# Performance work log

Hardware: AMD Instinct MI355X
Metric: run time of the kernel (lower is better)

Reference implementation:

```python
import jax, jax.numpy as jnp
import numpy as np

NUM_NEURONS = 8192
INPUT_SIZE = 512
OUTPUT_SIZE = 512
TAU = 10.0
G = 1.5


def setup_inputs() -> dict:
    key = jax.random.key(0)
    k1, k2, k3, k4, k5 = jax.random.split(key, 5)
    inputs = jax.random.normal(k1, (INPUT_SIZE,), dtype=jnp.float32)
    potentials = jax.random.normal(k2, (1, NUM_NEURONS), dtype=jnp.float32)
    # parameters, matching the torch init scales
    W_in = jax.random.normal(k3, (INPUT_SIZE, NUM_NEURONS), dtype=jnp.float32) * 0.1
    synapses = jax.random.normal(k4, (NUM_NEURONS, NUM_NEURONS), dtype=jnp.float32) / np.sqrt(NUM_NEURONS).astype(np.float32)
    W_out = jax.random.normal(k5, (NUM_NEURONS, OUTPUT_SIZE), dtype=jnp.float32) / np.float32(NUM_NEURONS)
    return {"inputs": inputs, "potentials": potentials, "W_in": W_in,
            "synapses": synapses, "W_out": W_out}


def reference(inputs, potentials, W_in, synapses, W_out):
    # input_map: bias-free linear, then unsqueeze to [1, N]
    drive = (inputs @ W_in)[None, :]                      # [1, N]
    # Neurons: continuous-time leaky integrator (FORCE-style)
    rates = jnp.tanh(potentials)                          # [1, N]
    pot_new = potentials + (-potentials + G * (rates @ synapses) + drive) / TAU
    gen_net = jnp.tanh(pot_new)                           # [1, N]
    # read_out: bias-free linear
    output = gen_net @ W_out                              # [1, output_size]
    return (output, pot_new)
```

## Files before the change

### kernel.cpp

```cpp
#include <hip/hip_runtime.h>
#include <math.h>

#define N_NEU   8192
#define IN_SZ   512
#define OUT_SZ  512
constexpr float TAU_INV = 0.1f;
constexpr float G_GAIN  = 1.5f;

__global__ void init_kernel(const float* __restrict__ pot,
                            float* __restrict__ rates,
                            float* __restrict__ drive,
                            float* __restrict__ y,
                            float* __restrict__ out_head) {
    int j = blockIdx.x * blockDim.x + threadIdx.x;
    if (j < N_NEU) {
        float p = pot[j];
        rates[j] = tanhf(p);
        drive[j] = 0.0f;
        y[j]     = 0.0f;
    }
    if (j < OUT_SZ) out_head[j] = 0.0f;
}

template<int KPB>
__global__ void gemv_acc(const float* __restrict__ x,
                         const float* __restrict__ M,
                         float* __restrict__ y,
                         int n4) {
    __shared__ float xs[KPB];
    const int k0 = blockIdx.y * KPB;
    for (int t = threadIdx.x; t < KPB; t += blockDim.x) xs[t] = x[k0 + t];
    __syncthreads();

    const int col4 = blockIdx.x * blockDim.x + threadIdx.x;
    const float4* Mp = (const float4*)M + (size_t)k0 * n4 + col4;

    float4 acc = make_float4(0.f, 0.f, 0.f, 0.f);
#pragma unroll 8
    for (int i = 0; i < KPB; ++i) {
        float  s = xs[i];
        float4 m = Mp[(size_t)i * n4];
        acc.x = fmaf(s, m.x, acc.x);
        acc.y = fmaf(s, m.y, acc.y);
        acc.z = fmaf(s, m.z, acc.z);
        acc.w = fmaf(s, m.w, acc.w);
    }

    float* yp = y + (size_t)col4 * 4;
    atomicAdd(yp + 0, acc.x);
    atomicAdd(yp + 1, acc.y);
    atomicAdd(yp + 2, acc.z);
    atomicAdd(yp + 3, acc.w);
}

__global__ void finalize_kernel(const float* __restrict__ pot,
                                const float* __restrict__ y,
                                const float* __restrict__ drive,
                                float* __restrict__ pot_out,
                                float* __restrict__ gen) {
    int j = blockIdx.x * blockDim.x + threadIdx.x;
    float p  = pot[j];
    float pn = p + (-p + G_GAIN * y[j] + drive[j]) * TAU_INV;
    pot_out[j] = pn;
    gen[j]     = tanhf(pn);
}

extern "C" void kernel_launch(void* const* d_in, const int* in_sizes, int n_in,
                              void* d_out, int out_size, void* d_ws, size_t ws_size,
                              hipStream_t stream) {
    const float* inputs   = (const float*)d_in[0];
    const float* pot      = (const float*)d_in[1];
    const float* W_in     = (const float*)d_in[2];
    const float* synapses = (const float*)d_in[3];
    const float* W_out    = (const float*)d_in[4];

    float* out = (float*)d_out;

    float* ws_rates = (float*)d_ws;
    float* ws_drive = ws_rates + N_NEU;
    float* ws_y     = ws_drive + N_NEU;
    float* ws_gen   = ws_y     + N_NEU;

    init_kernel<<<dim3(N_NEU / 256), dim3(256), 0, stream>>>(
        pot, ws_rates, ws_drive, ws_y, out);

    gemv_acc<16><<<dim3(N_NEU / 4 / 256, IN_SZ / 16), dim3(256), 0, stream>>>(
        inputs, W_in, ws_drive, N_NEU / 4);

    gemv_acc<128><<<dim3(N_NEU / 4 / 256, N_NEU / 128), dim3(256), 0, stream>>>(
        ws_rates, synapses, ws_y, N_NEU / 4);

    finalize_kernel<<<dim3(N_NEU / 256), dim3(256), 0, stream>>>(
        pot, ws_y, ws_drive, out + OUT_SZ, ws_gen);

    gemv_acc<32><<<dim3(1, N_NEU / 32), dim3(128), 0, stream>>>(
        ws_gen, W_out, out, OUT_SZ / 4);
}
```

Before: 419.0 us.

## Fuse pipeline into two kernels with merged W_in/synapse GEMV and fused finalize-readout

Collapses five launches into two memsets plus two kernels. The first kernel runs the W_in and synapse GEMVs in one grid, computing the scaled tanh rates inline and summing both into a single accumulator. The second kernel recomputes the potential update and tanh per block, then does the W_out readout and writes pot_new, with no intermediate gen buffer. This cuts launch overhead and round trips to intermediate buffers, and changes the synapse K-split (128→64), which doubles the number of atomics.

After: 407.6 us. 1.03x faster.

```diff
diff --git a/kernel.cpp b/kernel.cpp
--- a/kernel.cpp
+++ b/kernel.cpp
@@ -4,65 +4,97 @@
 #define N_NEU   8192
 #define IN_SZ   512
 #define OUT_SZ  512
+#define N4      (N_NEU / 4)
+#define KPB     64
 constexpr float TAU_INV = 0.1f;
 constexpr float G_GAIN  = 1.5f;
 
-__global__ void init_kernel(const float* __restrict__ pot,
-                            float* __restrict__ rates,
-                            float* __restrict__ drive,
-                            float* __restrict__ y,
-                            float* __restrict__ out_head) {
-    int j = blockIdx.x * blockDim.x + threadIdx.x;
-    if (j < N_NEU) {
-        float p = pot[j];
-        rates[j] = tanhf(p);
-        drive[j] = 0.0f;
-        y[j]     = 0.0f;
+__global__ __launch_bounds__(256)
+void accum_kernel(const float* __restrict__ pot,
+                  const float* __restrict__ inputs,
+                  const float* __restrict__ synapses,
+                  const float* __restrict__ W_in,
+                  float* __restrict__ acc_buf) {
+    __shared__ float xs[KPB];
+    const int by = blockIdx.y;
+    const float4* M;
+    int k0;
+    if (by < N_NEU / KPB) {
+        k0 = by * KPB;
+        M  = (const float4*)synapses;
+        if (threadIdx.x < KPB)
+            xs[threadIdx.x] = G_GAIN * tanhf(pot[k0 + threadIdx.x]);
+    } else {
+        k0 = (by - N_NEU / KPB) * KPB;
+        M  = (const float4*)W_in;
+        if (threadIdx.x < KPB)
+            xs[threadIdx.x] = inputs[k0 + threadIdx.x];
     }
-    if (j < OUT_SZ) out_head[j] = 0.0f;
-}
-
-template<int KPB>
-__global__ void gemv_acc(const float* __restrict__ x,
-                         const float* __restrict__ M,
-                         float* __restrict__ y,
-                         int n4) {
-    __shared__ float xs[KPB];
-    const int k0 = blockIdx.y * KPB;
-    for (int t = threadIdx.x; t < KPB; t += blockDim.x) xs[t] = x[k0 + t];
     __syncthreads();
 
     const int col4 = blockIdx.x * blockDim.x + threadIdx.x;
-    const float4* Mp = (const float4*)M + (size_t)k0 * n4 + col4;
+    const float4* Mp = M + (size_t)k0 * N4 + col4;
 
     float4 acc = make_float4(0.f, 0.f, 0.f, 0.f);
 #pragma unroll 8
     for (int i = 0; i < KPB; ++i) {
         float  s = xs[i];
-        float4 m = Mp[(size_t)i * n4];
+        float4 m = Mp[(size_t)i * N4];
         acc.x = fmaf(s, m.x, acc.x);
         acc.y = fmaf(s, m.y, acc.y);
         acc.z = fmaf(s, m.z, acc.z);
         acc.w = fmaf(s, m.w, acc.w);
     }
 
-    float* yp = y + (size_t)col4 * 4;
+    float* yp = acc_buf + (size_t)col4 * 4;
     atomicAdd(yp + 0, acc.x);
     atomicAdd(yp + 1, acc.y);
     atomicAdd(yp + 2, acc.z);
     atomicAdd(yp + 3, acc.w);
 }
 
-__global__ void finalize_kernel(const float* __restrict__ pot,
-                                const float* __restrict__ y,
-                                const float* __restrict__ drive,
-                                float* __restrict__ pot_out,
-                                float* __restrict__ gen) {
-    int j = blockIdx.x * blockDim.x + threadIdx.x;
-    float p  = pot[j];
-    float pn = p + (-p + G_GAIN * y[j] + drive[j]) * TAU_INV;
-    pot_out[j] = pn;
-    gen[j]     = tanhf(pn);
+#define K2_KPB   64
+#define OUT4     (OUT_SZ / 4)
+__global__ __launch_bounds__(128)
+void finish_kernel(const float* __restrict__ pot,
+                   const float* __restrict__ acc_buf,
+                   const float* __restrict__ W_out,
+                   float* __restrict__ out) {
+    const int b = blockIdx.x;
+    if (b < N_NEU / K2_KPB) {
+        __shared__ float xs[K2_KPB];
+        const int k0 = b * K2_KPB;
+        if (threadIdx.x < K2_KPB) {
+            int k = k0 + threadIdx.x;
+            float p  = pot[k];
+            float pn = p + (acc_buf[k] - p) * TAU_INV;
+            xs[threadIdx.x] = tanhf(pn);
+        }
+        __syncthreads();
+
+        const int col4 = threadIdx.x;
+        const float4* Wp = (const float4*)W_out + (size_t)k0 * OUT4 + col4;
+        float4 acc = make_float4(0.f, 0.f, 0.f, 0.f);
+#pragma unroll 8
+        for (int i = 0; i < K2_KPB; ++i) {
+            float  s = xs[i];
+            float4 m = Wp[(size_t)i * OUT4];
+            acc.x = fmaf(s, m.x, acc.x);
+            acc.y = fmaf(s, m.y, acc.y);
+            acc.z = fmaf(s, m.z, acc.z);
+            acc.w = fmaf(s, m.w, acc.w);
+        }
+        float* op = out + (size_t)col4 * 4;
+        atomicAdd(op + 0, acc.x);
+        atomicAdd(op + 1, acc.y);
+        atomicAdd(op + 2, acc.z);
+        atomicAdd(op + 3, acc.w);
+    } else {
+        int j = (b - N_NEU / K2_KPB) * 128 + threadIdx.x;
+        float p  = pot[j];
+        float pn = p + (acc_buf[j] - p) * TAU_INV;
+        out[OUT_SZ + j] = pn;
+    }
 }
 
 extern "C" void kernel_launch(void* const* d_in, const int* in_sizes, int n_in,
@@ -74,25 +106,15 @@
     const float* synapses = (const float*)d_in[3];
     const float* W_out    = (const float*)d_in[4];
 
-    float* out = (float*)d_out;
+    float* out     = (float*)d_out;
+    float* acc_buf = (float*)d_ws;
 
-    float* ws_rates = (float*)d_ws;
-    float* ws_drive = ws_rates + N_NEU;
-    float* ws_y     = ws_drive + N_NEU;
-    float* ws_gen   = ws_y     + N_NEU;
+    hipMemsetAsync(acc_buf, 0, N_NEU * sizeof(float), stream);
+    hipMemsetAsync(out, 0, OUT_SZ * sizeof(float), stream);
 
-    init_kernel<<<dim3(N_NEU / 256), dim3(256), 0, stream>>>(
-        pot, ws_rates, ws_drive, ws_y, out);
+    accum_kernel<<<dim3(N4 / 256, N_NEU / KPB + IN_SZ / KPB), dim3(256), 0, stream>>>(
+        pot, inputs, synapses, W_in, acc_buf);
 
-    gemv_acc<16><<<dim3(N_NEU / 4 / 256, IN_SZ / 16), dim3(256), 0, stream>>>(
-        inputs, W_in, ws_drive, N_NEU / 4);
-
-    gemv_acc<128><<<dim3(N_NEU / 4 / 256, N_NEU / 128), dim3(256), 0, stream>>>(
-        ws_rates, synapses, ws_y, N_NEU / 4);
-
-    finalize_kernel<<<dim3(N_NEU / 256), dim3(256), 0, stream>>>(
-        pot, ws_y, ws_drive, out + OUT_SZ, ws_gen);
-
-    gemv_acc<32><<<dim3(1, N_NEU / 32), dim3(128), 0, stream>>>(
-        ws_gen, W_out, out, OUT_SZ / 4);
+    finish_kernel<<<dim3(N_NEU / K2_KPB + N_NEU / 128), dim3(128), 0, stream>>>(
+        pot, acc_buf, W_out, out);
 }
```
